# Kernel optimization log

Hardware: AMD Instinct MI355X
Metric: run time of the kernel (lower is better)

Reference implementation:

```python
import jax, jax.numpy as jnp
import numpy as np

H = 8  # num attention heads

def _ln(x, g, b, eps=1e-5):
    m = jnp.mean(x, -1, keepdims=True)
    v = jnp.mean((x - m) ** 2, -1, keepdims=True)
    return (x - m) / jnp.sqrt(v + eps) * g + b

def _mha(x, Wqkv, bqkv, Wo, bo, bias=None):
    Bn, N, D = x.shape
    d = D // H
    q = (x @ Wqkv[0].T + bqkv[0]).reshape(Bn, N, H, d)
    k = (x @ Wqkv[1].T + bqkv[1]).reshape(Bn, N, H, d)
    v = (x @ Wqkv[2].T + bqkv[2]).reshape(Bn, N, H, d)
    s = jnp.einsum('bihd,bjhd->bhij', q, k) * (1.0 / np.sqrt(d))
    if bias is not None:
        s = s + jnp.transpose(bias, (0, 3, 1, 2))  # [Bn,H,N,N] additive bias
    a = jax.nn.softmax(s, axis=-1)
    o = jnp.einsum('bhij,bjhd->bihd', a, v).reshape(Bn, N, D)
    return o @ Wo.T + bo

def _ffn(x, W1, b1, W2, b2):
    return jax.nn.relu(x @ W1.T + b1) @ W2.T + b2

def _pe(T, dim):
    pos = jnp.arange(T, dtype=jnp.float32)[:, None]
    div = jnp.exp(jnp.arange(0, dim, 2, dtype=jnp.float32) * (-np.log(10000.0) / dim))
    pe = jnp.zeros((T, dim), jnp.float32)
    pe = pe.at[:, 0::2].set(jnp.sin(pos * div))
    pe = pe.at[:, 1::2].set(jnp.cos(pos * div))
    return pe

def reference(pose, W_pose, W_emb, prelu_a, W_bias, gWqkv, gbqkv, gWo, gbo, gln1g, gln1b, gW1, gb1, gW2, gb2, gln2g, gln2b, deW, deb, tWqkv, tbqkv, tWo, tbo, tln1g, tln1b, tW1, tb1, tW2, tb2, tln2g, tln2b, W_out):
    B, C, T, V = pose.shape
    D = W_pose.shape[0]
    p = jnp.transpose(pose, (0, 2, 3, 1))  # [B,T,V,C]
    y = jnp.einsum('btvc,dc->btvd', p, W_pose).reshape(B * T, V, D)
    bias_pre = p[:, :, None, :, :] - p[:, :, :, None, :]  # [B,T,V,V,C] pairwise diffs
    pe = _pe(T, D)
    for i in range(2):
        h = jnp.einsum('btijc,hc->btijh', bias_pre, W_emb[i])  # [B,T,V,V,256]
        h = jnp.where(h >= 0, h, prelu_a[i] * h)               # PReLU
        bias = (jnp.einsum('btijh,gh->btijg', h, W_bias[i]) * (1.0 / np.sqrt(float(H)))).reshape(B * T, V, V, H)
        # GraphEncoder: post-LN transformer block with additive per-head attn bias
        a = _mha(y, gWqkv[i], gbqkv[i], gWo[i], gbo[i], bias)
        y1 = _ln(y + a, gln1g[i], gln1b[i])
        g = _ln(y1 + _ffn(y1, gW1[i], gb1[i], gW2[i], gb2[i]), gln2g[i], gln2b[i])
        g = g @ deW[i].T + deb[i]                              # gat_de linear
        # torch .view(B*V, T, -1): raw memory reinterpretation -> jnp.reshape
        y = g.reshape(B * V, T, D) + pe[None]                  # positional encoding
        mem = y
        # temporal Encoder: post-LN transformer block, no bias
        a = _mha(y, tWqkv[i], tbqkv[i], tWo[i], tbo[i])
        y1 = _ln(y + a, tln1g[i], tln1b[i])
        y = _ln(y1 + _ffn(y1, tW1[i], tb1[i], tW2[i], tb2[i]), tln2g[i], tln2b[i])
        y = (y + mem).reshape(B * T, V, D)
    out = jnp.einsum('bvd,od->bvo', y, W_out)
    out = jnp.where(out >= 0, out, 0.01 * out)  # LeakyReLU
    return out.reshape(B, -1, T, V)

def setup_inputs() -> dict:
    key = jax.random.key(0)
    ks = iter(jax.random.split(key, 64))
    def g(shape, scale):
        return jax.random.normal(next(ks), shape, jnp.float32) * scale
    B, C, T, V = 16, 32, 62, 19
    D, Hd, O = 128, 256, 64
    inp = {
        'pose': g((B, C, T, V), 1.0),
        'W_pose': g((D, C), 1.0 / np.sqrt(C)),
        'W_emb': g((2, Hd, C), 1.0 / np.sqrt(C)),
        'prelu_a': jnp.full((2,), 0.25, jnp.float32),
        'W_bias': g((2, H, Hd), 1.0 / np.sqrt(Hd)),
        'gWqkv': g((2, 3, D, D), 1.0 / np.sqrt(D)),
        'gbqkv': jnp.zeros((2, 3, D), jnp.float32),
        'gWo': g((2, D, D), 1.0 / np.sqrt(D)),
        'gbo': jnp.zeros((2, D), jnp.float32),
        'gln1g': jnp.ones((2, D), jnp.float32), 'gln1b': jnp.zeros((2, D), jnp.float32),
        'gW1': g((2, Hd, D), 1.0 / np.sqrt(D)), 'gb1': jnp.zeros((2, Hd), jnp.float32),
        'gW2': g((2, D, Hd), 1.0 / np.sqrt(Hd)), 'gb2': jnp.zeros((2, D), jnp.float32),
        'gln2g': jnp.ones((2, D), jnp.float32), 'gln2b': jnp.zeros((2, D), jnp.float32),
        'deW': g((2, D, D), 1.0 / np.sqrt(D)), 'deb': jnp.zeros((2, D), jnp.float32),
        'tWqkv': g((2, 3, D, D), 1.0 / np.sqrt(D)),
        'tbqkv': jnp.zeros((2, 3, D), jnp.float32),
        'tWo': g((2, D, D), 1.0 / np.sqrt(D)),
        'tbo': jnp.zeros((2, D), jnp.float32),
        'tln1g': jnp.ones((2, D), jnp.float32), 'tln1b': jnp.zeros((2, D), jnp.float32),
        'tW1': g((2, Hd, D), 1.0 / np.sqrt(D)), 'tb1': jnp.zeros((2, Hd), jnp.float32),
        'tW2': g((2, D, Hd), 1.0 / np.sqrt(Hd)), 'tb2': jnp.zeros((2, D), jnp.float32),
        'tln2g': jnp.ones((2, D), jnp.float32), 'tln2b': jnp.zeros((2, D), jnp.float32),
        'W_out': g((O, D), 1.0 / np.sqrt(D)),
    }
    return inp
```

## Files before the change

kernel.cpp:

```cpp
#include <hip/hip_runtime.h>
#include <hip/hip_bf16.h>
#include <math.h>

#define B_  16
#define C_  32
#define T_  62
#define V_  19
#define D_  128
#define HD_ 256
#define H_  8
#define DH_ 16
#define ROWS 18848
#define RT_  1178
#define BT_ 992
#define BV_ 304

typedef __attribute__((ext_vector_type(8))) short short8v;
typedef __attribute__((ext_vector_type(4))) float f32x4;

struct alignas(8) bf4 { __hip_bfloat16 x, y, z, w; };

__global__ void transpose_kernel(const float* __restrict__ pose, __hip_bfloat16* __restrict__ p_bf) {
    int idx = blockIdx.x * 256 + threadIdx.x;
    if (idx >= B_ * T_ * V_ * C_) return;
    int c = idx & 31;
    int rest = idx >> 5;
    int v = rest % V_;
    int rest2 = rest / V_;
    int t = rest2 % T_;
    int b = rest2 / T_;
    p_bf[idx] = __float2bfloat16(pose[((size_t)((b * C_ + c) * T_ + t)) * V_ + v]);
}

__global__ void wconv_kernel(
        const float* s0, const float* s1, const float* s2, const float* s3,
        const float* s4, const float* s5, const float* s6, const float* s7,
        const float* s8, const float* s9, const float* s10, const float* s11,
        __hip_bfloat16* __restrict__ dst) {
    int idx = blockIdx.x * 256 + threadIdx.x;
    if (idx >= 585728) return;
    const float* s; int base;
    if      (idx <   4096) { s = s0;  base = 0;      }
    else if (idx <  20480) { s = s1;  base = 4096;   }
    else if (idx < 118784) { s = s2;  base = 20480;  }
    else if (idx < 151552) { s = s3;  base = 118784; }
    else if (idx < 217088) { s = s4;  base = 151552; }
    else if (idx < 282624) { s = s5;  base = 217088; }
    else if (idx < 315392) { s = s6;  base = 282624; }
    else if (idx < 413696) { s = s7;  base = 315392; }
    else if (idx < 446464) { s = s8;  base = 413696; }
    else if (idx < 512000) { s = s9;  base = 446464; }
    else if (idx < 577536) { s = s10; base = 512000; }
    else                   { s = s11; base = 577536; }
    dst[idx] = __float2bfloat16(s[idx - base]);
}

__global__ __launch_bounds__(512) void w2_kernel(
        const float* __restrict__ Wbias, const float* __restrict__ Wemb,
        float* __restrict__ w2) {
    int tid = threadIdx.x;
    int layer = tid >> 8, g = (tid >> 5) & 7, c = tid & 31;
    float acc = 0.f;
    for (int hh = 0; hh < HD_; ++hh)
        acc += Wbias[layer * 2048 + g * HD_ + hh] * Wemb[layer * 8192 + hh * C_ + c];
    w2[layer * 256 + g * C_ + c] = acc;
}

template<int N, int K, int EPI, bool HASBIAS, bool O32, bool O16>
__global__ __launch_bounds__(256) void mfma_linear(
        const __hip_bfloat16* __restrict__ A, const __hip_bfloat16* __restrict__ W,
        const float* __restrict__ bias, float* __restrict__ out32,
        __hip_bfloat16* __restrict__ out16) {
    int wave = threadIdx.x >> 6;
    int lane = threadIdx.x & 63;
    int rt = blockIdx.x;
    int nt = blockIdx.y * 4 + wave;
    int r0 = rt * 16, n0 = nt * 16;
    int rl = lane & 15;
    int kk = (lane >> 4) * 8;
    const short* Ab = (const short*)A + (size_t)(r0 + rl) * K + kk;
    const short* Wb = (const short*)W + (size_t)(n0 + rl) * K + kk;
    f32x4 acc = {0.f, 0.f, 0.f, 0.f};
    #pragma unroll
    for (int kb = 0; kb < K / 32; ++kb) {
        short8v a = *reinterpret_cast<const short8v*>(Ab + kb * 32);
        short8v b = *reinterpret_cast<const short8v*>(Wb + kb * 32);
        acc = __builtin_amdgcn_mfma_f32_16x16x32_bf16(a, b, acc, 0, 0, 0);
    }
    int oc = n0 + rl;
    int or0 = r0 + (lane >> 4) * 4;
    float bv = HASBIAS ? bias[oc] : 0.f;
    float freq = 0.f;
    if (EPI == 3) freq = expf(-(float)(oc & ~1) * (9.210340371976184f / 128.f));
    #pragma unroll
    for (int j = 0; j < 4; ++j) {
        float v = acc[j] + bv;
        if (EPI == 1) v = fmaxf(v, 0.f);
        if (EPI == 2) v = v >= 0.f ? v : 0.01f * v;
        if (EPI == 3) {
            int t = (or0 + j) % T_;
            float ang = (float)t * freq;
            v += (oc & 1) ? cosf(ang) : sinf(ang);
        }
        if (O32) out32[(size_t)(or0 + j) * N + oc] = v;
        if (O16) out16[(size_t)(or0 + j) * N + oc] = __float2bfloat16(v);
    }
}

__global__ __launch_bounds__(256) void bias2_kernel(
        const float* __restrict__ e, const __hip_bfloat16* __restrict__ p_bf,
        const float* __restrict__ prelu_a, const float* __restrict__ Wbias,
        const float* __restrict__ w2, float* __restrict__ bias) {
    int bt = blockIdx.x;
    __shared__ float es[V_ * 257];
    __shared__ float ps[V_ * 33];
    __shared__ float f_lds[V_ * 8];
    int tid = threadIdx.x;
    for (int idx = tid; idx < V_ * 64; idx += 256) {
        int v = idx >> 6, h4 = idx & 63;
        float4 val = *reinterpret_cast<const float4*>(
            &e[((size_t)(bt * V_ + v)) * HD_ + h4 * 4]);
        float* d = &es[v * 257 + h4 * 4];
        d[0] = val.x; d[1] = val.y; d[2] = val.z; d[3] = val.w;
    }
    if (tid < V_ * 8) {
        int v = tid >> 3, c4 = (tid & 7) * 4;
        bf4 pv = *reinterpret_cast<const bf4*>(&p_bf[((size_t)(bt * V_ + v)) * C_ + c4]);
        float* d = &ps[v * 33 + c4];
        d[0] = __bfloat162float(pv.x); d[1] = __bfloat162float(pv.y);
        d[2] = __bfloat162float(pv.z); d[3] = __bfloat162float(pv.w);
    }
    __syncthreads();
    if (tid < V_ * 8) {
        int v = tid >> 3, g = tid & 7;
        const float* pr = &ps[v * 33];
        const float* wr = &w2[g * C_];
        float acc = 0.f;
        #pragma unroll
        for (int c = 0; c < C_; ++c) acc += pr[c] * wr[c];
        f_lds[v * 8 + g] = acc;
    }
    __syncthreads();
    if (tid < 190) {
        int i = 0, rem = tid, cnt = V_;
        while (rem >= cnt) { rem -= cnt; ++i; --cnt; }
        int j = i + rem;
        const float a = prelu_a[0];
        const float scale = 0.35355339059327373f;
        const float cL = 0.5f * (1.f + a) * scale;
        const float cA = 0.5f * (1.f - a) * scale;
        const float* ei = es + i * 257;
        const float* ej = es + j * 257;
        float S[H_] = {0.f, 0.f, 0.f, 0.f, 0.f, 0.f, 0.f, 0.f};
        #pragma unroll 4
        for (int hh = 0; hh < HD_; ++hh) {
            float d = ej[hh] - ei[hh];
            float ad = fabsf(d);
            const float* w = Wbias + hh;
            #pragma unroll
            for (int g = 0; g < H_; ++g) S[g] += w[g * HD_] * ad;
        }
        float* bij = bias + ((size_t)bt * (V_ * V_) + i * V_ + j) * H_;
        float* bji = bias + ((size_t)bt * (V_ * V_) + j * V_ + i) * H_;
        #pragma unroll
        for (int g = 0; g < H_; ++g) {
            float lin = cL * (f_lds[j * 8 + g] - f_lds[i * 8 + g]);
            float sym = cA * S[g];
            bij[g] = lin + sym;
            bji[g] = sym - lin;
        }
    }
}

__global__ __launch_bounds__(384) void attn_graph_kernel(
        const float* __restrict__ qkv, const float* __restrict__ bias,
        __hip_bfloat16* __restrict__ out) {
    int bt = blockIdx.x;
    int h = blockIdx.y;
    __shared__ float q_lds[V_][20];
    __shared__ float k_lds[V_][20];
    __shared__ float v_lds[V_][20];
    __shared__ float sm[V_][20];
    int tid = threadIdx.x;
    for (int idx = tid; idx < V_ * 4 * 3; idx += 384) {
        int mat = idx / (V_ * 4);
        int rem = idx - mat * (V_ * 4);
        int row = rem >> 2, part = rem & 3;
        float4 val = *reinterpret_cast<const float4*>(
            qkv + ((size_t)(bt * V_ + row)) * 384 + mat * 128 + h * DH_ + part * 4);
        float* dst = (mat == 0 ? q_lds[row] : (mat == 1 ? k_lds[row] : v_lds[row])) + part * 4;
        *reinterpret_cast<float4*>(dst) = val;
    }
    __syncthreads();
    if (tid < V_ * V_) {
        int i = tid / V_, j = tid - i * V_;
        float acc = 0.f;
        #pragma unroll
        for (int c = 0; c < 4; ++c) {
            float4 qv = *reinterpret_cast<const float4*>(&q_lds[i][4 * c]);
            float4 kv = *reinterpret_cast<const float4*>(&k_lds[j][4 * c]);
            acc += qv.x * kv.x + qv.y * kv.y + qv.z * kv.z + qv.w * kv.w;
        }
        sm[i][j] = acc * 0.25f + bias[((size_t)(bt * V_ + i) * V_ + j) * H_ + h];
    }
    __syncthreads();
    if (tid < V_) {
        float m = -1e30f;
        for (int j = 0; j < V_; ++j) m = fmaxf(m, sm[tid][j]);
        float sum = 0.f;
        for (int j = 0; j < V_; ++j) { float e = __expf(sm[tid][j] - m); sm[tid][j] = e; sum += e; }
        float inv = 1.f / sum;
        for (int j = 0; j < V_; ++j) sm[tid][j] *= inv;
    }
    __syncthreads();
    if (tid < V_ * DH_) {
        int i = tid / DH_, d = tid - i * DH_;
        float o = 0.f;
        #pragma unroll 4
        for (int j = 0; j < V_; ++j) o += sm[i][j] * v_lds[j][d];
        out[((size_t)(bt * V_ + i)) * D_ + h * DH_ + d] = __float2bfloat16(o);
    }
}

__global__ __launch_bounds__(256) void attn_temporal_kernel(
        const float* __restrict__ qkv, __hip_bfloat16* __restrict__ out) {
    int b = blockIdx.x;
    int h = blockIdx.y;
    __shared__ float q_lds[T_][20];
    __shared__ float k_lds[T_][20];
    __shared__ float v_lds[T_][20];
    __shared__ float sm[T_][68];
    int tid = threadIdx.x;
    for (int idx = tid; idx < T_ * 4 * 3; idx += 256) {
        int mat = idx / (T_ * 4);
        int rem = idx - mat * (T_ * 4);
        int row = rem >> 2, part = rem & 3;
        float4 val = *reinterpret_cast<const float4*>(
            qkv + ((size_t)(b * T_ + row)) * 384 + mat * 128 + h * DH_ + part * 4);
        float* dst = (mat == 0 ? q_lds[row] : (mat == 1 ? k_lds[row] : v_lds[row])) + part * 4;
        *reinterpret_cast<float4*>(dst) = val;
    }
    __syncthreads();
    if (tid < T_ * 4) {
        int i = tid >> 2, jt = tid & 3;
        float qreg[16];
        #pragma unroll
        for (int c = 0; c < 4; ++c) {
            float4 qv = *reinterpret_cast<const float4*>(&q_lds[i][4 * c]);
            qreg[4 * c + 0] = qv.x * 0.25f;
            qreg[4 * c + 1] = qv.y * 0.25f;
            qreg[4 * c + 2] = qv.z * 0.25f;
            qreg[4 * c + 3] = qv.w * 0.25f;
        }
        float s[16];
        #pragma unroll
        for (int jj = 0; jj < 16; ++jj) {
            int j = jj * 4 + jt;
            float acc = -1e30f;
            if (j < T_) {
                acc = 0.f;
                const float* kr = k_lds[j];
                #pragma unroll
                for (int c = 0; c < 4; ++c) {
                    float4 kv = *reinterpret_cast<const float4*>(&kr[4 * c]);
                    acc += qreg[4*c+0] * kv.x + qreg[4*c+1] * kv.y
                         + qreg[4*c+2] * kv.z + qreg[4*c+3] * kv.w;
                }
            }
            s[jj] = acc;
        }
        float m = -1e30f;
        #pragma unroll
        for (int jj = 0; jj < 16; ++jj) m = fmaxf(m, s[jj]);
        m = fmaxf(m, __shfl_xor(m, 1, 64));
        m = fmaxf(m, __shfl_xor(m, 2, 64));
        float sum = 0.f;
        #pragma unroll
        for (int jj = 0; jj < 16; ++jj) {
            int j = jj * 4 + jt;
            float e = (j < T_) ? __expf(s[jj] - m) : 0.f;
            s[jj] = e;
            sum += e;
        }
        sum += __shfl_xor(sum, 1, 64);
        sum += __shfl_xor(sum, 2, 64);
        float inv = 1.f / sum;
        #pragma unroll
        for (int jj = 0; jj < 16; ++jj) {
            int j = jj * 4 + jt;
            if (j < T_) sm[i][j] = s[jj] * inv;
        }
    }
    __syncthreads();
    if (tid < T_ * 4) {
        int i = tid >> 2, dg = tid & 3;
        float4 o = {0.f, 0.f, 0.f, 0.f};
        for (int j = 0; j < T_; ++j) {
            float pp = sm[i][j];
            const float4 vv = *reinterpret_cast<const float4*>(&v_lds[j][4 * dg]);
            o.x += pp * vv.x; o.y += pp * vv.y; o.z += pp * vv.z; o.w += pp * vv.w;
        }
        bf4 ov = { __float2bfloat16(o.x), __float2bfloat16(o.y),
                   __float2bfloat16(o.z), __float2bfloat16(o.w) };
        *reinterpret_cast<bf4*>(out + ((size_t)(b * T_ + i)) * D_ + h * DH_ + 4 * dg) = ov;
    }
}

template<bool O32, bool O16>
__global__ __launch_bounds__(64) void ln_add_kernel(
        const float* __restrict__ x, const float* __restrict__ r,
        const float* __restrict__ g, const float* __restrict__ b,
        float* __restrict__ o32, __hip_bfloat16* __restrict__ o16) {
    int row = blockIdx.x;
    int lane = threadIdx.x;
    const float* xr = x + (size_t)row * D_;
    const float* rr = r + (size_t)row * D_;
    float v0 = xr[lane] + rr[lane];
    float v1 = xr[lane + 64] + rr[lane + 64];
    float s = v0 + v1, sq = v0 * v0 + v1 * v1;
    #pragma unroll
    for (int off = 32; off > 0; off >>= 1) {
        s += __shfl_xor(s, off, 64);
        sq += __shfl_xor(sq, off, 64);
    }
    float mean = s * (1.f / 128.f);
    float var = sq * (1.f / 128.f) - mean * mean;
    float rstd = rsqrtf(var + 1e-5f);
    float a0 = (v0 - mean) * rstd * g[lane]      + b[lane];
    float a1 = (v1 - mean) * rstd * g[lane + 64] + b[lane + 64];
    if (O32) {
        float* o = o32 + (size_t)row * D_;
        o[lane] = a0; o[lane + 64] = a1;
    }
    if (O16) {
        __hip_bfloat16* o = o16 + (size_t)row * D_;
        o[lane] = __float2bfloat16(a0); o[lane + 64] = __float2bfloat16(a1);
    }
}

__global__ __launch_bounds__(64) void ln_add_add_kernel(
        const float* __restrict__ x, const float* __restrict__ r,
        const float* __restrict__ g, const float* __restrict__ b,
        float* __restrict__ y, __hip_bfloat16* __restrict__ y_bf) {
    int row = blockIdx.x;
    int lane = threadIdx.x;
    const float* xr = x + (size_t)row * D_;
    const float* rr = r + (size_t)row * D_;
    float v0 = xr[lane] + rr[lane];
    float v1 = xr[lane + 64] + rr[lane + 64];
    float s = v0 + v1, sq = v0 * v0 + v1 * v1;
    #pragma unroll
    for (int off = 32; off > 0; off >>= 1) {
        s += __shfl_xor(s, off, 64);
        sq += __shfl_xor(sq, off, 64);
    }
    float mean = s * (1.f / 128.f);
    float var = sq * (1.f / 128.f) - mean * mean;
    float rstd = rsqrtf(var + 1e-5f);
    float a0 = (v0 - mean) * rstd * g[lane]      + b[lane];
    float a1 = (v1 - mean) * rstd * g[lane + 64] + b[lane + 64];
    float* yp = y + (size_t)row * D_;
    __hip_bfloat16* yb = y_bf + (size_t)row * D_;
    float y0 = yp[lane] + a0;
    float y1v = yp[lane + 64] + a1;
    yp[lane] = y0;       yb[lane] = __float2bfloat16(y0);
    yp[lane + 64] = y1v; yb[lane + 64] = __float2bfloat16(y1v);
}

extern "C" void kernel_launch(void* const* d_in, const int* in_sizes, int n_in,
                              void* d_out, int out_size, void* d_ws, size_t ws_size,
                              hipStream_t stream) {
    const float* pose    = (const float*)d_in[0];
    const float* W_pose  = (const float*)d_in[1];
    const float* W_emb   = (const float*)d_in[2];
    const float* prelu_a = (const float*)d_in[3];
    const float* W_bias  = (const float*)d_in[4];
    const float* gWqkv   = (const float*)d_in[5];
    const float* gbqkv   = (const float*)d_in[6];
    const float* gWo     = (const float*)d_in[7];
    const float* gbo     = (const float*)d_in[8];
    const float* gln1g   = (const float*)d_in[9];
    const float* gln1b   = (const float*)d_in[10];
    const float* gW1     = (const float*)d_in[11];
    const float* gb1     = (const float*)d_in[12];
    const float* gW2     = (const float*)d_in[13];
    const float* gb2     = (const float*)d_in[14];
    const float* gln2g   = (const float*)d_in[15];
    const float* gln2b   = (const float*)d_in[16];
    const float* deW     = (const float*)d_in[17];
    const float* deb     = (const float*)d_in[18];
    const float* tWqkv   = (const float*)d_in[19];
    const float* tbqkv   = (const float*)d_in[20];
    const float* tWo     = (const float*)d_in[21];
    const float* tbo     = (const float*)d_in[22];
    const float* tln1g   = (const float*)d_in[23];
    const float* tln1b   = (const float*)d_in[24];
    const float* tW1     = (const float*)d_in[25];
    const float* tb1     = (const float*)d_in[26];
    const float* tW2     = (const float*)d_in[27];
    const float* tb2     = (const float*)d_in[28];
    const float* tln2g   = (const float*)d_in[29];
    const float* tln2b   = (const float*)d_in[30];
    const float* W_out   = (const float*)d_in[31];

    float* ws = (float*)d_ws;
    __hip_bfloat16* p_bf   = (__hip_bfloat16*)(ws + 0);
    float*          y      = ws + 301568;
    __hip_bfloat16* y_bf   = (__hip_bfloat16*)(ws + 2714112);
    float*          biasbuf= ws + 3920384;
    float*          big    = ws + 6785280;
    float*          e      = big;
    float*          qkvf   = big;
    float*          tmp    = big;
    __hip_bfloat16* hid_bf = (__hip_bfloat16*)(big + 2412544);
    float*          y1     = big + 4825088;
    __hip_bfloat16* attn_bf= (__hip_bfloat16*)(ws + 14022912);
    float*          t2     = ws + 15229184;
    __hip_bfloat16* y1_bf  = (__hip_bfloat16*)t2;
    __hip_bfloat16* t2_bf  = (__hip_bfloat16*)t2;
    __hip_bfloat16* w_bf   = (__hip_bfloat16*)(ws + 17641728);
    float*          w2     = ws + 17934592;
    float*          outf   = (float*)d_out;

    const int oWpose = 0, oWemb = 4096, oGqkv = 20480, oGwo = 118784, oGw1 = 151552,
              oGw2 = 217088, oDe = 282624, oTqkv = 315392, oTwo = 413696,
              oTw1 = 446464, oTw2 = 512000, oWout = 577536;

    wconv_kernel<<<(585728 + 255) / 256, 256, 0, stream>>>(
        W_pose, W_emb, gWqkv, gWo, gW1, gW2, deW, tWqkv, tWo, tW1, tW2, W_out, w_bf);
    w2_kernel<<<1, 512, 0, stream>>>(W_bias, W_emb, w2);
    transpose_kernel<<<(B_*T_*V_*C_ + 255) / 256, 256, 0, stream>>>(pose, p_bf);
    mfma_linear<128, 32, 0, false, true, true><<<dim3(RT_, 2), 256, 0, stream>>>(
        p_bf, w_bf + oWpose, nullptr, y, y_bf);

    for (int i = 0; i < 2; ++i) {
        mfma_linear<256, 32, 0, false, true, false><<<dim3(RT_, 4), 256, 0, stream>>>(
            p_bf, w_bf + oWemb + i * 8192, nullptr, e, nullptr);
        bias2_kernel<<<BT_, 256, 0, stream>>>(
            e, p_bf, prelu_a + i, W_bias + (size_t)i * H_ * HD_, w2 + i * 256, biasbuf);
        mfma_linear<384, 128, 0, true, true, false><<<dim3(RT_, 6), 256, 0, stream>>>(
            y_bf, w_bf + oGqkv + i * 49152, gbqkv + (size_t)i * 384, qkvf, nullptr);
        attn_graph_kernel<<<dim3(BT_, H_), 384, 0, stream>>>(qkvf, biasbuf, attn_bf);
        mfma_linear<128, 128, 0, true, true, false><<<dim3(RT_, 2), 256, 0, stream>>>(
            attn_bf, w_bf + oGwo + i * 16384, gbo + (size_t)i * D_, tmp, nullptr);
        ln_add_kernel<true, true><<<ROWS, 64, 0, stream>>>(
            y, tmp, gln1g + (size_t)i * D_, gln1b + (size_t)i * D_, y1, y1_bf);
        mfma_linear<256, 128, 1, true, false, true><<<dim3(RT_, 4), 256, 0, stream>>>(
            y1_bf, w_bf + oGw1 + i * 32768, gb1 + (size_t)i * HD_, nullptr, hid_bf);
        mfma_linear<128, 256, 0, true, true, false><<<dim3(RT_, 2), 256, 0, stream>>>(
            hid_bf, w_bf + oGw2 + i * 32768, gb2 + (size_t)i * D_, tmp, nullptr);
        ln_add_kernel<false, true><<<ROWS, 64, 0, stream>>>(
            y1, tmp, gln2g + (size_t)i * D_, gln2b + (size_t)i * D_, nullptr, t2_bf);
        mfma_linear<128, 128, 3, true, true, true><<<dim3(RT_, 2), 256, 0, stream>>>(
            t2_bf, w_bf + oDe + i * 16384, deb + (size_t)i * D_, y, y_bf);

        mfma_linear<384, 128, 0, true, true, false><<<dim3(RT_, 6), 256, 0, stream>>>(
            y_bf, w_bf + oTqkv + i * 49152, tbqkv + (size_t)i * 384, qkvf, nullptr);
        attn_temporal_kernel<<<dim3(BV_, H_), 256, 0, stream>>>(qkvf, attn_bf);
        mfma_linear<128, 128, 0, true, true, false><<<dim3(RT_, 2), 256, 0, stream>>>(
            attn_bf, w_bf + oTwo + i * 16384, tbo + (size_t)i * D_, tmp, nullptr);
        ln_add_kernel<true, true><<<ROWS, 64, 0, stream>>>(
            y, tmp, tln1g + (size_t)i * D_, tln1b + (size_t)i * D_, y1, y1_bf);
        mfma_linear<256, 128, 1, true, false, true><<<dim3(RT_, 4), 256, 0, stream>>>(
            y1_bf, w_bf + oTw1 + i * 32768, tb1 + (size_t)i * HD_, nullptr, hid_bf);
        mfma_linear<128, 256, 0, true, true, false><<<dim3(RT_, 2), 256, 0, stream>>>(
            hid_bf, w_bf + oTw2 + i * 32768, tb2 + (size_t)i * D_, tmp, nullptr);
        ln_add_add_kernel<<<ROWS, 64, 0, stream>>>(
            y1, tmp, tln2g + (size_t)i * D_, tln2b + (size_t)i * D_, y, y_bf);
    }

    mfma_linear<64, 128, 2, false, true, false><<<dim3(RT_, 1), 256, 0, stream>>>(
        y_bf, w_bf + oWout, nullptr, outf, nullptr);
}
```

Measured before the change: 738.4 us.

## Switch linears to 32x32 MFMA tiles and fuse W_emb projection into bias kernel

```diff
diff --git a/kernel.cpp b/kernel.cpp
--- a/kernel.cpp
+++ b/kernel.cpp
@@ -11,12 +11,13 @@
 #define H_  8
 #define DH_ 16
 #define ROWS 18848
-#define RT_  1178
+#define RT32_ 589
 #define BT_ 992
 #define BV_ 304
 
 typedef __attribute__((ext_vector_type(8))) short short8v;
 typedef __attribute__((ext_vector_type(4))) float f32x4;
+typedef __attribute__((ext_vector_type(16))) float f32x16;
 
 struct alignas(8) bf4 { __hip_bfloat16 x, y, z, w; };
 
@@ -73,42 +74,43 @@
         __hip_bfloat16* __restrict__ out16) {
     int wave = threadIdx.x >> 6;
     int lane = threadIdx.x & 63;
-    int rt = blockIdx.x;
     int nt = blockIdx.y * 4 + wave;
-    int r0 = rt * 16, n0 = nt * 16;
-    int rl = lane & 15;
-    int kk = (lane >> 4) * 8;
+    int n0 = nt * 32;
+    if (n0 >= N) return;
+    int r0 = blockIdx.x * 32;
+    int rl = lane & 31;
+    int kk = (lane >> 5) * 8;
     const short* Ab = (const short*)A + (size_t)(r0 + rl) * K + kk;
     const short* Wb = (const short*)W + (size_t)(n0 + rl) * K + kk;
-    f32x4 acc = {0.f, 0.f, 0.f, 0.f};
+    f32x16 acc = {0.f,0.f,0.f,0.f,0.f,0.f,0.f,0.f,0.f,0.f,0.f,0.f,0.f,0.f,0.f,0.f};
     #pragma unroll
-    for (int kb = 0; kb < K / 32; ++kb) {
-        short8v a = *reinterpret_cast<const short8v*>(Ab + kb * 32);
-        short8v b = *reinterpret_cast<const short8v*>(Wb + kb * 32);
-        acc = __builtin_amdgcn_mfma_f32_16x16x32_bf16(a, b, acc, 0, 0, 0);
+    for (int kb = 0; kb < K / 16; ++kb) {
+        short8v a = *reinterpret_cast<const short8v*>(Ab + kb * 16);
+        short8v b = *reinterpret_cast<const short8v*>(Wb + kb * 16);
+        acc = __builtin_amdgcn_mfma_f32_32x32x16_bf16(a, b, acc, 0, 0, 0);
     }
     int oc = n0 + rl;
-    int or0 = r0 + (lane >> 4) * 4;
     float bv = HASBIAS ? bias[oc] : 0.f;
     float freq = 0.f;
     if (EPI == 3) freq = expf(-(float)(oc & ~1) * (9.210340371976184f / 128.f));
     #pragma unroll
-    for (int j = 0; j < 4; ++j) {
-        float v = acc[j] + bv;
+    for (int reg = 0; reg < 16; ++reg) {
+        int orow = r0 + (reg & 3) + 8 * (reg >> 2) + 4 * (lane >> 5);
+        float v = acc[reg] + bv;
         if (EPI == 1) v = fmaxf(v, 0.f);
         if (EPI == 2) v = v >= 0.f ? v : 0.01f * v;
         if (EPI == 3) {
-            int t = (or0 + j) % T_;
+            int t = orow % T_;
             float ang = (float)t * freq;
             v += (oc & 1) ? cosf(ang) : sinf(ang);
         }
-        if (O32) out32[(size_t)(or0 + j) * N + oc] = v;
-        if (O16) out16[(size_t)(or0 + j) * N + oc] = __float2bfloat16(v);
+        if (O32) out32[(size_t)orow * N + oc] = v;
+        if (O16) out16[(size_t)orow * N + oc] = __float2bfloat16(v);
     }
 }
 
 __global__ __launch_bounds__(256) void bias2_kernel(
-        const float* __restrict__ e, const __hip_bfloat16* __restrict__ p_bf,
+        const __hip_bfloat16* __restrict__ p_bf, const __hip_bfloat16* __restrict__ wemb_bf,
         const float* __restrict__ prelu_a, const float* __restrict__ Wbias,
         const float* __restrict__ w2, float* __restrict__ bias) {
     int bt = blockIdx.x;
@@ -116,13 +118,6 @@
     __shared__ float ps[V_ * 33];
     __shared__ float f_lds[V_ * 8];
     int tid = threadIdx.x;
-    for (int idx = tid; idx < V_ * 64; idx += 256) {
-        int v = idx >> 6, h4 = idx & 63;
-        float4 val = *reinterpret_cast<const float4*>(
-            &e[((size_t)(bt * V_ + v)) * HD_ + h4 * 4]);
-        float* d = &es[v * 257 + h4 * 4];
-        d[0] = val.x; d[1] = val.y; d[2] = val.z; d[3] = val.w;
-    }
     if (tid < V_ * 8) {
         int v = tid >> 3, c4 = (tid & 7) * 4;
         bf4 pv = *reinterpret_cast<const bf4*>(&p_bf[((size_t)(bt * V_ + v)) * C_ + c4]);
@@ -131,6 +126,25 @@
         d[2] = __bfloat162float(pv.z); d[3] = __bfloat162float(pv.w);
     }
     __syncthreads();
+    {
+        float wr[C_];
+        const __hip_bfloat16* wrow = wemb_bf + (size_t)tid * C_;
+        #pragma unroll
+        for (int c4 = 0; c4 < 8; ++c4) {
+            bf4 wv = *reinterpret_cast<const bf4*>(wrow + c4 * 4);
+            wr[c4 * 4 + 0] = __bfloat162float(wv.x);
+            wr[c4 * 4 + 1] = __bfloat162float(wv.y);
+            wr[c4 * 4 + 2] = __bfloat162float(wv.z);
+            wr[c4 * 4 + 3] = __bfloat162float(wv.w);
+        }
+        for (int v = 0; v < V_; ++v) {
+            const float* pr = &ps[v * 33];
+            float acc = 0.f;
+            #pragma unroll
+            for (int c = 0; c < C_; ++c) acc += pr[c] * wr[c];
+            es[v * 257 + tid] = acc;
+        }
+    }
     if (tid < V_ * 8) {
         int v = tid >> 3, g = tid & 7;
         const float* pr = &ps[v * 33];
@@ -409,7 +423,6 @@
     __hip_bfloat16* y_bf   = (__hip_bfloat16*)(ws + 2714112);
     float*          biasbuf= ws + 3920384;
     float*          big    = ws + 6785280;
-    float*          e      = big;
     float*          qkvf   = big;
     float*          tmp    = big;
     __hip_bfloat16* hid_bf = (__hip_bfloat16*)(big + 2412544);
@@ -430,45 +443,44 @@
         W_pose, W_emb, gWqkv, gWo, gW1, gW2, deW, tWqkv, tWo, tW1, tW2, W_out, w_bf);
     w2_kernel<<<1, 512, 0, stream>>>(W_bias, W_emb, w2);
     transpose_kernel<<<(B_*T_*V_*C_ + 255) / 256, 256, 0, stream>>>(pose, p_bf);
-    mfma_linear<128, 32, 0, false, true, true><<<dim3(RT_, 2), 256, 0, stream>>>(
+    mfma_linear<128, 32, 0, false, true, true><<<dim3(RT32_, 1), 256, 0, stream>>>(
         p_bf, w_bf + oWpose, nullptr, y, y_bf);
 
     for (int i = 0; i < 2; ++i) {
-        mfma_linear<256, 32, 0, false, true, false><<<dim3(RT_, 4), 256, 0, stream>>>(
-            p_bf, w_bf + oWemb + i * 8192, nullptr, e, nullptr);
         bias2_kernel<<<BT_, 256, 0, stream>>>(
-            e, p_bf, prelu_a + i, W_bias + (size_t)i * H_ * HD_, w2 + i * 256, biasbuf);
-        mfma_linear<384, 128, 0, true, true, false><<<dim3(RT_, 6), 256, 0, stream>>>(
+            p_bf, w_bf + oWemb + i * 8192, prelu_a + i,
+            W_bias + (size_t)i * H_ * HD_, w2 + i * 256, biasbuf);
+        mfma_linear<384, 128, 0, true, true, false><<<dim3(RT32_, 3), 256, 0, stream>>>(
             y_bf, w_bf + oGqkv + i * 49152, gbqkv + (size_t)i * 384, qkvf, nullptr);
         attn_graph_kernel<<<dim3(BT_, H_), 384, 0, stream>>>(qkvf, biasbuf, attn_bf);
-        mfma_linear<128, 128, 0, true, true, false><<<dim3(RT_, 2), 256, 0, stream>>>(
+        mfma_linear<128, 128, 0, true, true, false><<<dim3(RT32_, 1), 256, 0, stream>>>(
             attn_bf, w_bf + oGwo + i * 16384, gbo + (size_t)i * D_, tmp, nullptr);
         ln_add_kernel<true, true><<<ROWS, 64, 0, stream>>>(
             y, tmp, gln1g + (size_t)i * D_, gln1b + (size_t)i * D_, y1, y1_bf);
-        mfma_linear<256, 128, 1, true, false, true><<<dim3(RT_, 4), 256, 0, stream>>>(
+        mfma_linear<256, 128, 1, true, false, true><<<dim3(RT32_, 2), 256, 0, stream>>>(
             y1_bf, w_bf + oGw1 + i * 32768, gb1 + (size_t)i * HD_, nullptr, hid_bf);
-        mfma_linear<128, 256, 0, true, true, false><<<dim3(RT_, 2), 256, 0, stream>>>(
+        mfma_linear<128, 256, 0, true, true, false><<<dim3(RT32_, 1), 256, 0, stream>>>(
             hid_bf, w_bf + oGw2 + i * 32768, gb2 + (size_t)i * D_, tmp, nullptr);
         ln_add_kernel<false, true><<<ROWS, 64, 0, stream>>>(
             y1, tmp, gln2g + (size_t)i * D_, gln2b + (size_t)i * D_, nullptr, t2_bf);
-        mfma_linear<128, 128, 3, true, true, true><<<dim3(RT_, 2), 256, 0, stream>>>(
+        mfma_linear<128, 128, 3, true, true, true><<<dim3(RT32_, 1), 256, 0, stream>>>(
             t2_bf, w_bf + oDe + i * 16384, deb + (size_t)i * D_, y, y_bf);
 
-        mfma_linear<384, 128, 0, true, true, false><<<dim3(RT_, 6), 256, 0, stream>>>(
+        mfma_linear<384, 128, 0, true, true, false><<<dim3(RT32_, 3), 256, 0, stream>>>(
             y_bf, w_bf + oTqkv + i * 49152, tbqkv + (size_t)i * 384, qkvf, nullptr);
         attn_temporal_kernel<<<dim3(BV_, H_), 256, 0, stream>>>(qkvf, attn_bf);
-        mfma_linear<128, 128, 0, true, true, false><<<dim3(RT_, 2), 256, 0, stream>>>(
+        mfma_linear<128, 128, 0, true, true, false><<<dim3(RT32_, 1), 256, 0, stream>>>(
             attn_bf, w_bf + oTwo + i * 16384, tbo + (size_t)i * D_, tmp, nullptr);
         ln_add_kernel<true, true><<<ROWS, 64, 0, stream>>>(
             y, tmp, tln1g + (size_t)i * D_, tln1b + (size_t)i * D_, y1, y1_bf);
-        mfma_linear<256, 128, 1, true, false, true><<<dim3(RT_, 4), 256, 0, stream>>>(
+        mfma_linear<256, 128, 1, true, false, true><<<dim3(RT32_, 2), 256, 0, stream>>>(
             y1_bf, w_bf + oTw1 + i * 32768, tb1 + (size_t)i * HD_, nullptr, hid_bf);
-        mfma_linear<128, 256, 0, true, true, false><<<dim3(RT_, 2), 256, 0, stream>>>(
+        mfma_linear<128, 256, 0, true, true, false><<<dim3(RT32_, 1), 256, 0, stream>>>(
             hid_bf, w_bf + oTw2 + i * 32768, tb2 + (size_t)i * D_, tmp, nullptr);
         ln_add_add_kernel<<<ROWS, 64, 0, stream>>>(
             y1, tmp, tln2g + (size_t)i * D_, tln2b + (size_t)i * D_, y, y_bf);
     }
 
-    mfma_linear<64, 128, 2, false, true, false><<<dim3(RT_, 1), 256, 0, stream>>>(
+    mfma_linear<64, 128, 2, false, true, false><<<dim3(RT32_, 1), 256, 0, stream>>>(
         y_bf, w_bf + oWout, nullptr, outf, nullptr);
 }
```

New measurement: 628.2 us. 14.9% less time.
